# Optimization experiments

Hardware: AMD Instinct MI355X
Metric: run time of the kernel (lower is better)

The kernel has to match this reference:

```python
import jax, jax.numpy as jnp
import numpy as np

DECAY = 0.8
COMMITMENT_WEIGHT = 1.0
EPS = 1e-5


def setup_inputs() -> dict:
    key = jax.random.key(0)
    k1, k2, k3 = jax.random.split(key, 3)
    B, T, D, K = 16, 2048, 512, 8192
    x = jax.random.normal(k1, (B, T, D), dtype=jnp.float32)
    embed = jax.random.normal(k2, (D, K), dtype=jnp.float32)
    cluster_size = jnp.ones((K,), dtype=jnp.float32)
    embed_avg = jax.random.normal(k3, (D, K), dtype=jnp.float32)
    return {"x": x, "embed": embed, "cluster_size": cluster_size, "embed_avg": embed_avg}


def reference(x, embed, cluster_size, embed_avg):
    B, T, D = x.shape
    K = embed.shape[1]
    flat = x.reshape(-1, D)  # [N, D]

    # squared L2 distance to each code: ||f||^2 - 2 f.e + ||e||^2  -> [N, K]
    dist = (flat * flat).sum(-1, keepdims=True) \
        - 2.0 * (flat @ embed) \
        + (embed * embed).sum(0, keepdims=True)
    embed_ind = jnp.argmin(dist, axis=1)  # [N] (== argmax of -dist)

    quantize = jnp.take(embed.T, embed_ind, axis=0).reshape(B, T, D)

    # ---- EMA codebook statistics (training-mode buffer updates) ----
    onehot_sum = jnp.zeros((K,), dtype=flat.dtype).at[embed_ind].add(1.0)  # [K]
    # flat.T @ onehot == segment-sum of tokens per code, transposed -> [D, K]
    embed_sum = jax.ops.segment_sum(flat, embed_ind, num_segments=K).T
    new_cluster_size = cluster_size * DECAY + (1.0 - DECAY) * onehot_sum
    new_embed_avg = embed_avg * DECAY + (1.0 - DECAY) * embed_sum
    n = new_cluster_size.sum()
    cs = (new_cluster_size + EPS) / (n + K * EPS) * n
    new_embed = new_embed_avg / cs[None, :]
    # (random re-init of unused codes is omitted: non-deterministic side effect)

    commitment_loss = jnp.mean((jax.lax.stop_gradient(quantize) - x) ** 2) * COMMITMENT_WEIGHT
    quantize_st = x + jax.lax.stop_gradient(quantize - x)  # straight-through

    return (quantize_st, embed_ind.reshape(B, T), commitment_loss,
            new_embed, new_cluster_size, new_embed_avg)
```

## Files before the change

kernel.cpp:

```cpp
#include <hip/hip_runtime.h>

#define NTOK   32768
#define DDIM   512
#define KCODES 8192
#define DK     (DDIM * KCODES)
#define DECAYF 0.8f
#define EPSF   1e-5f

using short8 = __attribute__((ext_vector_type(8))) short;
using f32x4  = __attribute__((ext_vector_type(4))) float;

#define WS_ESUMT  0
#define WS_ONEHOT DK
#define WS_ENORM  (DK + 8192)
#define WS_SCAL   (DK + 16384)
#define WS_PART   (WS_SCAL + 64)
#define WS_EHI    (WS_PART + 2 * NTOK)
#define WS_ELO    (WS_EHI + DK / 2)

__device__ __forceinline__ unsigned short bf16rne(float f) {
  unsigned u = __float_as_uint(f);
  unsigned r = u + 0x7FFFu + ((u >> 16) & 1u);
  return (unsigned short)(r >> 16);
}

__device__ __forceinline__ void gload_lds16(const unsigned short* g, unsigned short* l) {
  __builtin_amdgcn_global_load_lds(
      (const __attribute__((address_space(1))) unsigned int*)g,
      (__attribute__((address_space(3))) unsigned int*)l, 16, 0, 0);
}

__global__ __launch_bounds__(256) void prep_kernel(
    const float* __restrict__ x, const float* __restrict__ embed,
    const float* __restrict__ cluster_size,
    unsigned short* __restrict__ xhi, unsigned short* __restrict__ xlo,
    unsigned short* __restrict__ ehi, unsigned short* __restrict__ elo,
    float* __restrict__ e_norm, float* __restrict__ esumT,
    float* __restrict__ onehot, float* __restrict__ scal,
    unsigned long long* __restrict__ partials) {
  __shared__ float tile[32][33];
  __shared__ float part[8][32];
  __shared__ float w[4];
  const int bid = blockIdx.x;
  const int tid = threadIdx.x;

  if (bid < 8192) {
    const size_t i = ((size_t)bid * 256 + tid) * 8;
    const float4 v0 = *(const float4*)&x[i];
    const float4 v1 = *(const float4*)&x[i + 4];
    const float v[8] = {v0.x, v0.y, v0.z, v0.w, v1.x, v1.y, v1.z, v1.w};
    unsigned short h[8], l[8];
#pragma unroll
    for (int j = 0; j < 8; ++j) {
      h[j] = bf16rne(v[j]);
      l[j] = bf16rne(v[j] - __uint_as_float((unsigned)h[j] << 16));
    }
    uint4 H, L;
    H.x = h[0] | ((unsigned)h[1] << 16); H.y = h[2] | ((unsigned)h[3] << 16);
    H.z = h[4] | ((unsigned)h[5] << 16); H.w = h[6] | ((unsigned)h[7] << 16);
    L.x = l[0] | ((unsigned)l[1] << 16); L.y = l[2] | ((unsigned)l[3] << 16);
    L.z = l[4] | ((unsigned)l[5] << 16); L.w = l[6] | ((unsigned)l[7] << 16);
    *(uint4*)&xhi[i] = H;
    *(uint4*)&xlo[i] = L;
  } else if (bid < 8192 + 256) {
    const int k0 = (bid - 8192) * 32;
    const int tx = tid & 31;
    const int ty = tid >> 5;
    float sq = 0.f;
#pragma unroll 1
    for (int d0 = 0; d0 < DDIM; d0 += 32) {
      __syncthreads();
#pragma unroll
      for (int j = 0; j < 4; ++j) {
        const int dl = ty + j * 8;
        const float v = embed[(size_t)(d0 + dl) * KCODES + k0 + tx];
        tile[dl][tx] = v;
        sq += v * v;
      }
      __syncthreads();
#pragma unroll
      for (int j = 0; j < 4; ++j) {
        const int kl = ty + j * 8;
        const size_t idx = (size_t)(k0 + kl) * DDIM + d0 + tx;
        const float v = tile[tx][kl];
        const unsigned short h = bf16rne(v);
        ehi[idx] = h;
        elo[idx] = bf16rne(v - __uint_as_float((unsigned)h << 16));
      }
    }
    part[ty][tx] = sq;
    __syncthreads();
    if (ty == 0) {
      float s = 0.f;
#pragma unroll
      for (int j = 0; j < 8; ++j) s += part[j][tx];
      e_norm[k0 + tx] = s;
    }
  } else if (bid < 8192 + 256 + 2048) {
    const int zb = bid - (8192 + 256);
    const size_t off = (size_t)zb * 2048 + (size_t)tid * 8;
    const float4 z = {0.f, 0.f, 0.f, 0.f};
    *(float4*)&esumT[off] = z;
    *(float4*)&esumT[off + 4] = z;
  } else {
    const int b = bid - (8192 + 256 + 2048);
    onehot[b * 256 + tid] = 0.f;
    const size_t pbase = (size_t)b * 1024 + (size_t)tid * 4;
    const ulonglong2 ff = {~0ull, ~0ull};
    *(ulonglong2*)&partials[pbase] = ff;
    *(ulonglong2*)&partials[pbase + 2] = ff;
    float s = cluster_size[b * 256 + tid];
#pragma unroll
    for (int off = 32; off > 0; off >>= 1) s += __shfl_down(s, off);
    if ((tid & 63) == 0) w[tid >> 6] = s;
    __syncthreads();
    if (tid == 0) {
      scal[2 + b] = w[0] + w[1] + w[2] + w[3];
      if (b == 0) { scal[0] = 0.f; scal[1] = 0.f; }
    }
  }
}

__global__ __launch_bounds__(256) void argmin_mfma_kernel(
    const unsigned short* __restrict__ xhi, const unsigned short* __restrict__ xlo,
    const unsigned short* __restrict__ ehi, const unsigned short* __restrict__ elo,
    const float* __restrict__ e_norm, unsigned long long* __restrict__ partials) {
  __shared__ unsigned short Ahs[128 * 32];
  __shared__ unsigned short Als[128 * 32];
  __shared__ unsigned short Bhs[128 * 32];
  __shared__ unsigned short Bls[128 * 32];

  const int t    = threadIdx.x;
  const int wid  = t >> 6;
  const int lid  = t & 63;
  const int kblk = blockIdx.x;
  const int tokbase = blockIdx.y * 128;
  const int kbase   = kblk * 128;

  const int wrow = wid >> 1, wcol = wid & 1;
  const int m16  = lid & 15, kq = lid >> 4;

  const int srow = lid >> 2;
  const int gcol = ((lid & 3) ^ ((srow >> 1) & 3)) * 8;
  const int fsw = (kq ^ ((m16 >> 1) & 3)) * 8;

  f32x4 acc[4][4];
#pragma unroll
  for (int i = 0; i < 4; ++i)
#pragma unroll
    for (int j = 0; j < 4; ++j) acc[i][j] = (f32x4)0.f;

  const unsigned short* Ahg = xhi + (size_t)tokbase * DDIM;
  const unsigned short* Alg = xlo + (size_t)tokbase * DDIM;
  const unsigned short* Bhg = ehi + (size_t)kbase * DDIM;
  const unsigned short* Blg = elo + (size_t)kbase * DDIM;

#pragma unroll 1
  for (int d0 = 0; d0 < DDIM; d0 += 32) {
    __syncthreads();
#pragma unroll
    for (int p = 0; p < 2; ++p) {
      const int chunk = wid + p * 4;
      const size_t go = (size_t)(chunk * 16 + srow) * DDIM + d0 + gcol;
      gload_lds16(Ahg + go, &Ahs[chunk * 512]);
      gload_lds16(Alg + go, &Als[chunk * 512]);
      gload_lds16(Bhg + go, &Bhs[chunk * 512]);
      gload_lds16(Blg + go, &Bls[chunk * 512]);
    }
    __syncthreads();
    short8 bh[4], bl[4];
#pragma unroll
    for (int j = 0; j < 4; ++j) {
      const int r = (wcol * 64 + j * 16 + m16) * 32 + fsw;
      bh[j] = *(const short8*)&Bhs[r];
      bl[j] = *(const short8*)&Bls[r];
    }
#pragma unroll
    for (int i = 0; i < 4; ++i) {
      const int r = (wrow * 64 + i * 16 + m16) * 32 + fsw;
      const short8 ah = *(const short8*)&Ahs[r];
      const short8 al = *(const short8*)&Als[r];
#pragma unroll
      for (int j = 0; j < 4; ++j) {
        acc[i][j] = __builtin_amdgcn_mfma_f32_16x16x32_bf16(ah, bh[j], acc[i][j], 0, 0, 0);
        acc[i][j] = __builtin_amdgcn_mfma_f32_16x16x32_bf16(ah, bl[j], acc[i][j], 0, 0, 0);
        acc[i][j] = __builtin_amdgcn_mfma_f32_16x16x32_bf16(al, bh[j], acc[i][j], 0, 0, 0);
      }
    }
  }

  float en[4];
#pragma unroll
  for (int j = 0; j < 4; ++j)
    en[j] = e_norm[kbase + wcol * 64 + j * 16 + m16];

  __syncthreads();
  unsigned long long* red = (unsigned long long*)Ahs;
#pragma unroll
  for (int i = 0; i < 4; ++i) {
#pragma unroll
    for (int r = 0; r < 4; ++r) {
      unsigned long long best = 0xFFFFFFFFFFFFFFFFull;
#pragma unroll
      for (int j = 0; j < 4; ++j) {
        const float s = en[j] - 2.0f * acc[i][j][r];
        unsigned u = __float_as_uint(s);
        u = (u & 0x80000000u) ? ~u : (u | 0x80000000u);
        const unsigned k = (unsigned)(kbase + wcol * 64 + j * 16 + m16);
        const unsigned long long c = ((unsigned long long)u << 32) | k;
        best = (c < best) ? c : best;
      }
#pragma unroll
      for (int s = 1; s < 16; s <<= 1) {
        const unsigned long long c = __shfl_xor(best, s);
        best = (c < best) ? c : best;
      }
      if (m16 == 0)
        red[(wrow * 64 + i * 16 + kq * 4 + r) * 2 + wcol] = best;
    }
  }
  __syncthreads();
  if (t < 128) {
    const unsigned long long a0 = red[t * 2], a1 = red[t * 2 + 1];
    const unsigned long long m = (a0 < a1) ? a0 : a1;
    atomicMin(&partials[tokbase + t], m);
  }
}

__global__ __launch_bounds__(256) void gather_stats_kernel(
    const float* __restrict__ x, const unsigned short* __restrict__ ehi,
    const unsigned short* __restrict__ elo,
    const unsigned long long* __restrict__ partials,
    float* __restrict__ quant_out, float* __restrict__ indf_out,
    float* __restrict__ embed_sumT, float* __restrict__ onehot,
    float* __restrict__ scal) {
  const int sub = threadIdx.x >> 7;
  const int t7  = threadIdx.x & 127;
  const int n   = blockIdx.x * 2 + sub;
  __shared__ int s_ind[2];
  __shared__ float wsum[4];
  if (t7 == 0) {
    const int k = (int)(partials[n] & 0xFFFFFFFFull);
    s_ind[sub] = k;
    indf_out[n] = (float)k;
    atomicAdd(&onehot[k], 1.0f);
  }
  __syncthreads();
  const int k = s_ind[sub];
  const int d4 = t7 * 4;
  const ushort4 h4 = *(const ushort4*)&ehi[(size_t)k * DDIM + d4];
  const ushort4 l4 = *(const ushort4*)&elo[(size_t)k * DDIM + d4];
  float4 e;
  e.x = __uint_as_float((unsigned)h4.x << 16) + __uint_as_float((unsigned)l4.x << 16);
  e.y = __uint_as_float((unsigned)h4.y << 16) + __uint_as_float((unsigned)l4.y << 16);
  e.z = __uint_as_float((unsigned)h4.z << 16) + __uint_as_float((unsigned)l4.z << 16);
  e.w = __uint_as_float((unsigned)h4.w << 16) + __uint_as_float((unsigned)l4.w << 16);
  const float4 xv = *(const float4*)&x[(size_t)n * DDIM + d4];
  *(float4*)&quant_out[(size_t)n * DDIM + d4] = e;
  atomicAdd(&embed_sumT[(size_t)k * DDIM + d4 + 0], xv.x);
  atomicAdd(&embed_sumT[(size_t)k * DDIM + d4 + 1], xv.y);
  atomicAdd(&embed_sumT[(size_t)k * DDIM + d4 + 2], xv.z);
  atomicAdd(&embed_sumT[(size_t)k * DDIM + d4 + 3], xv.w);
  const float dx0 = e.x - xv.x, dx1 = e.y - xv.y, dx2 = e.z - xv.z, dx3 = e.w - xv.w;
  float ls = dx0 * dx0 + dx1 * dx1 + dx2 * dx2 + dx3 * dx3;
#pragma unroll
  for (int off = 32; off > 0; off >>= 1) ls += __shfl_down(ls, off);
  if ((threadIdx.x & 63) == 0) wsum[threadIdx.x >> 6] = ls;
  __syncthreads();
  if (threadIdx.x == 0)
    atomicAdd(&scal[0], wsum[0] + wsum[1] + wsum[2] + wsum[3]);
}

__global__ __launch_bounds__(256) void finalize_kernel(
    const float* __restrict__ embed_avg, const float* __restrict__ embed_sumT,
    const float* __restrict__ cluster_size, const float* __restrict__ onehot,
    const float* __restrict__ scal,
    float* __restrict__ out_embed, float* __restrict__ out_avg,
    float* __restrict__ out_ncs, float* __restrict__ out_loss) {
  __shared__ float tile[32][33];
  __shared__ float sh_nsum;
  const int k0 = blockIdx.x * 32;
  const int d0 = blockIdx.y * 32;
  const int tx = threadIdx.x & 31;
  const int ty = threadIdx.x >> 5;
  if (threadIdx.x == 0) {
    float s = 0.f;
#pragma unroll
    for (int b = 0; b < 32; ++b) s += scal[2 + b];
    sh_nsum = DECAYF * s + (1.0f - DECAYF) * (float)NTOK;
  }
#pragma unroll
  for (int j = 0; j < 4; ++j) {
    const int kl = ty + j * 8;
    tile[kl][tx] = embed_sumT[(size_t)(k0 + kl) * DDIM + d0 + tx];
  }
  __syncthreads();
  const float nsum = sh_nsum;
  const float ncs = DECAYF * cluster_size[k0 + tx] + (1.0f - DECAYF) * onehot[k0 + tx];
  const float csv = (ncs + EPSF) / (nsum + (float)KCODES * EPSF) * nsum;
#pragma unroll
  for (int j = 0; j < 4; ++j) {
    const int dl = ty + j * 8;
    const size_t idx = (size_t)(d0 + dl) * KCODES + k0 + tx;
    const float nea = DECAYF * embed_avg[idx] + (1.0f - DECAYF) * tile[tx][dl];
    out_avg[idx] = nea;
    out_embed[idx] = nea / csv;
  }
  if (blockIdx.y == 0 && ty == 0)
    out_ncs[k0 + tx] = ncs;
  if (blockIdx.x == 0 && blockIdx.y == 0 && threadIdx.x == 0)
    out_loss[0] = scal[0] * (1.0f / ((float)NTOK * (float)DDIM));
}

extern "C" void kernel_launch(void* const* d_in, const int* in_sizes, int n_in,
                              void* d_out, int out_size, void* d_ws, size_t ws_size,
                              hipStream_t stream) {
  (void)in_sizes; (void)n_in; (void)out_size; (void)ws_size;
  const float* x            = (const float*)d_in[0];
  const float* embed        = (const float*)d_in[1];
  const float* cluster_size = (const float*)d_in[2];
  const float* embed_avg    = (const float*)d_in[3];

  float* out = (float*)d_out;
  float* out_quant = out;
  float* out_indf  = out + 16777216;
  float* out_loss  = out + 16777216 + 32768;
  float* out_embed = out + 16777216 + 32768 + 1;
  float* out_ncs   = out_embed + DK;
  float* out_avg   = out_ncs + KCODES;

  float* ws = (float*)d_ws;
  float* esumT  = ws + WS_ESUMT;
  float* onehot = ws + WS_ONEHOT;
  float* e_norm = ws + WS_ENORM;
  float* scal   = ws + WS_SCAL;
  unsigned long long* partials = (unsigned long long*)(ws + WS_PART);
  unsigned short* ehi = (unsigned short*)(ws + WS_EHI);
  unsigned short* elo = (unsigned short*)(ws + WS_ELO);

  unsigned short* xhi = (unsigned short*)d_out;
  unsigned short* xlo = xhi + (size_t)NTOK * DDIM;

  prep_kernel<<<8192 + 256 + 2048 + 32, 256, 0, stream>>>(
      x, embed, cluster_size, xhi, xlo, ehi, elo, e_norm, esumT, onehot, scal, partials);

  argmin_mfma_kernel<<<dim3(64, 256), 256, 0, stream>>>(
      xhi, xlo, ehi, elo, e_norm, partials);

  gather_stats_kernel<<<NTOK / 2, 256, 0, stream>>>(
      x, ehi, elo, partials, out_quant, out_indf, esumT, onehot, scal);

  finalize_kernel<<<dim3(KCODES / 32, DDIM / 32), 256, 0, stream>>>(
      embed_avg, esumT, cluster_size, onehot, scal,
      out_embed, out_avg, out_ncs, out_loss);
}
```

Before: 1.382 ms.

## Fuse gather/stats into argmin via last-block counter; move quantize write to finalize

```diff
diff --git a/kernel.cpp b/kernel.cpp
--- a/kernel.cpp
+++ b/kernel.cpp
@@ -14,7 +14,8 @@
 #define WS_ONEHOT DK
 #define WS_ENORM  (DK + 8192)
 #define WS_SCAL   (DK + 16384)
-#define WS_PART   (WS_SCAL + 64)
+#define WS_CNT    (WS_SCAL + 64)
+#define WS_PART   (WS_CNT + 256)
 #define WS_EHI    (WS_PART + 2 * NTOK)
 #define WS_ELO    (WS_EHI + DK / 2)
 
@@ -22,6 +23,10 @@
   unsigned u = __float_as_uint(f);
   unsigned r = u + 0x7FFFu + ((u >> 16) & 1u);
   return (unsigned short)(r >> 16);
+}
+
+__device__ __forceinline__ float bf2f(unsigned short h) {
+  return __uint_as_float((unsigned)h << 16);
 }
 
 __device__ __forceinline__ void gload_lds16(const unsigned short* g, unsigned short* l) {
@@ -37,7 +42,7 @@
     unsigned short* __restrict__ ehi, unsigned short* __restrict__ elo,
     float* __restrict__ e_norm, float* __restrict__ esumT,
     float* __restrict__ onehot, float* __restrict__ scal,
-    unsigned long long* __restrict__ partials) {
+    unsigned* __restrict__ cnt, unsigned long long* __restrict__ partials) {
   __shared__ float tile[32][33];
   __shared__ float part[8][32];
   __shared__ float w[4];
@@ -53,7 +58,7 @@
 #pragma unroll
     for (int j = 0; j < 8; ++j) {
       h[j] = bf16rne(v[j]);
-      l[j] = bf16rne(v[j] - __uint_as_float((unsigned)h[j] << 16));
+      l[j] = bf16rne(v[j] - bf2f(h[j]));
     }
     uint4 H, L;
     H.x = h[0] | ((unsigned)h[1] << 16); H.y = h[2] | ((unsigned)h[3] << 16);
@@ -85,7 +90,7 @@
         const float v = tile[tx][kl];
         const unsigned short h = bf16rne(v);
         ehi[idx] = h;
-        elo[idx] = bf16rne(v - __uint_as_float((unsigned)h << 16));
+        elo[idx] = bf16rne(v - bf2f(h));
       }
     }
     part[ty][tx] = sq;
@@ -109,6 +114,7 @@
     const ulonglong2 ff = {~0ull, ~0ull};
     *(ulonglong2*)&partials[pbase] = ff;
     *(ulonglong2*)&partials[pbase + 2] = ff;
+    if (b == 0) cnt[tid] = 0u;
     float s = cluster_size[b * 256 + tid];
 #pragma unroll
     for (int off = 32; off > 0; off >>= 1) s += __shfl_down(s, off);
@@ -124,7 +130,10 @@
 __global__ __launch_bounds__(256) void argmin_mfma_kernel(
     const unsigned short* __restrict__ xhi, const unsigned short* __restrict__ xlo,
     const unsigned short* __restrict__ ehi, const unsigned short* __restrict__ elo,
-    const float* __restrict__ e_norm, unsigned long long* __restrict__ partials) {
+    const float* __restrict__ e_norm, unsigned long long* __restrict__ partials,
+    const float* __restrict__ x, float* __restrict__ indf_out,
+    float* __restrict__ onehot, float* __restrict__ esumT,
+    float* __restrict__ scal, unsigned* __restrict__ cnt) {
   __shared__ unsigned short Ahs[128 * 32];
   __shared__ unsigned short Als[128 * 32];
   __shared__ unsigned short Bhs[128 * 32];
@@ -225,64 +234,91 @@
     const unsigned long long m = (a0 < a1) ? a0 : a1;
     atomicMin(&partials[tokbase + t], m);
   }
-}
-
-__global__ __launch_bounds__(256) void gather_stats_kernel(
-    const float* __restrict__ x, const unsigned short* __restrict__ ehi,
-    const unsigned short* __restrict__ elo,
-    const unsigned long long* __restrict__ partials,
-    float* __restrict__ quant_out, float* __restrict__ indf_out,
-    float* __restrict__ embed_sumT, float* __restrict__ onehot,
-    float* __restrict__ scal) {
-  const int sub = threadIdx.x >> 7;
-  const int t7  = threadIdx.x & 127;
-  const int n   = blockIdx.x * 2 + sub;
-  __shared__ int s_ind[2];
-  __shared__ float wsum[4];
-  if (t7 == 0) {
-    const int k = (int)(partials[n] & 0xFFFFFFFFull);
-    s_ind[sub] = k;
-    indf_out[n] = (float)k;
-    atomicAdd(&onehot[k], 1.0f);
-  }
-  __syncthreads();
-  const int k = s_ind[sub];
-  const int d4 = t7 * 4;
-  const ushort4 h4 = *(const ushort4*)&ehi[(size_t)k * DDIM + d4];
-  const ushort4 l4 = *(const ushort4*)&elo[(size_t)k * DDIM + d4];
-  float4 e;
-  e.x = __uint_as_float((unsigned)h4.x << 16) + __uint_as_float((unsigned)l4.x << 16);
-  e.y = __uint_as_float((unsigned)h4.y << 16) + __uint_as_float((unsigned)l4.y << 16);
-  e.z = __uint_as_float((unsigned)h4.z << 16) + __uint_as_float((unsigned)l4.z << 16);
-  e.w = __uint_as_float((unsigned)h4.w << 16) + __uint_as_float((unsigned)l4.w << 16);
-  const float4 xv = *(const float4*)&x[(size_t)n * DDIM + d4];
-  *(float4*)&quant_out[(size_t)n * DDIM + d4] = e;
-  atomicAdd(&embed_sumT[(size_t)k * DDIM + d4 + 0], xv.x);
-  atomicAdd(&embed_sumT[(size_t)k * DDIM + d4 + 1], xv.y);
-  atomicAdd(&embed_sumT[(size_t)k * DDIM + d4 + 2], xv.z);
-  atomicAdd(&embed_sumT[(size_t)k * DDIM + d4 + 3], xv.w);
-  const float dx0 = e.x - xv.x, dx1 = e.y - xv.y, dx2 = e.z - xv.z, dx3 = e.w - xv.w;
-  float ls = dx0 * dx0 + dx1 * dx1 + dx2 * dx2 + dx3 * dx3;
-#pragma unroll
-  for (int off = 32; off > 0; off >>= 1) ls += __shfl_down(ls, off);
-  if ((threadIdx.x & 63) == 0) wsum[threadIdx.x >> 6] = ls;
-  __syncthreads();
-  if (threadIdx.x == 0)
-    atomicAdd(&scal[0], wsum[0] + wsum[1] + wsum[2] + wsum[3]);
+
+  __threadfence();
+  __syncthreads();
+  int* s_last = (int*)Als;
+  float* gred = (float*)(Als + 16);
+  if (t == 0) {
+    const unsigned v = atomicAdd(&cnt[blockIdx.y], 1u);
+    *s_last = (v == 63u);
+  }
+  __syncthreads();
+  if (*s_last) {
+    __threadfence();
+    float ls = 0.f;
+#pragma unroll 1
+    for (int i = 0; i < 32; ++i) {
+      const int n = tokbase + i * 4 + wid;
+      unsigned long long pv = 0ull;
+      if (lid == 0) pv = atomicAdd(&partials[n], 0ull);
+      int k = (int)(pv & 0xFFFFFFFFull);
+      k = __shfl(k, 0);
+      if (lid == 0) {
+        indf_out[n] = (float)k;
+        atomicAdd(&onehot[k], 1.0f);
+      }
+      const int d8 = lid * 8;
+      const float4 xv0 = *(const float4*)&x[(size_t)n * DDIM + d8];
+      const float4 xv1 = *(const float4*)&x[(size_t)n * DDIM + d8 + 4];
+      const ushort4 h0 = *(const ushort4*)&ehi[(size_t)k * DDIM + d8];
+      const ushort4 h1 = *(const ushort4*)&ehi[(size_t)k * DDIM + d8 + 4];
+      const ushort4 l0 = *(const ushort4*)&elo[(size_t)k * DDIM + d8];
+      const ushort4 l1 = *(const ushort4*)&elo[(size_t)k * DDIM + d8 + 4];
+      const float xv[8] = {xv0.x, xv0.y, xv0.z, xv0.w, xv1.x, xv1.y, xv1.z, xv1.w};
+      const float ev[8] = {
+          bf2f(h0.x) + bf2f(l0.x), bf2f(h0.y) + bf2f(l0.y),
+          bf2f(h0.z) + bf2f(l0.z), bf2f(h0.w) + bf2f(l0.w),
+          bf2f(h1.x) + bf2f(l1.x), bf2f(h1.y) + bf2f(l1.y),
+          bf2f(h1.z) + bf2f(l1.z), bf2f(h1.w) + bf2f(l1.w)};
+#pragma unroll
+      for (int j = 0; j < 8; ++j) {
+        atomicAdd(&esumT[(size_t)k * DDIM + d8 + j], xv[j]);
+        const float dx = ev[j] - xv[j];
+        ls += dx * dx;
+      }
+    }
+#pragma unroll
+    for (int off = 32; off > 0; off >>= 1) ls += __shfl_down(ls, off);
+    if (lid == 0) gred[wid] = ls;
+    __syncthreads();
+    if (t == 0) atomicAdd(&scal[0], gred[0] + gred[1] + gred[2] + gred[3]);
+  }
 }
 
 __global__ __launch_bounds__(256) void finalize_kernel(
     const float* __restrict__ embed_avg, const float* __restrict__ embed_sumT,
     const float* __restrict__ cluster_size, const float* __restrict__ onehot,
-    const float* __restrict__ scal,
+    const float* __restrict__ scal, const unsigned long long* __restrict__ partials,
+    const unsigned short* __restrict__ ehi, const unsigned short* __restrict__ elo,
     float* __restrict__ out_embed, float* __restrict__ out_avg,
-    float* __restrict__ out_ncs, float* __restrict__ out_loss) {
+    float* __restrict__ out_ncs, float* __restrict__ out_loss,
+    float* __restrict__ out_quant) {
   __shared__ float tile[32][33];
   __shared__ float sh_nsum;
   const int k0 = blockIdx.x * 32;
   const int d0 = blockIdx.y * 32;
   const int tx = threadIdx.x & 31;
   const int ty = threadIdx.x >> 5;
+
+  {
+    const int nbase = (blockIdx.y * 256 + blockIdx.x) * 8;
+    const int n = nbase + (threadIdx.x >> 5);
+    const int k = (int)(partials[n] & 0xFFFFFFFFull);
+    const int d16 = (threadIdx.x & 31) * 16;
+#pragma unroll
+    for (int c = 0; c < 4; ++c) {
+      const ushort4 h4 = *(const ushort4*)&ehi[(size_t)k * DDIM + d16 + c * 4];
+      const ushort4 l4 = *(const ushort4*)&elo[(size_t)k * DDIM + d16 + c * 4];
+      float4 e;
+      e.x = bf2f(h4.x) + bf2f(l4.x);
+      e.y = bf2f(h4.y) + bf2f(l4.y);
+      e.z = bf2f(h4.z) + bf2f(l4.z);
+      e.w = bf2f(h4.w) + bf2f(l4.w);
+      *(float4*)&out_quant[(size_t)n * DDIM + d16 + c * 4] = e;
+    }
+  }
+
   if (threadIdx.x == 0) {
     float s = 0.f;
 #pragma unroll
@@ -334,6 +370,7 @@
   float* onehot = ws + WS_ONEHOT;
   float* e_norm = ws + WS_ENORM;
   float* scal   = ws + WS_SCAL;
+  unsigned* cnt = (unsigned*)(ws + WS_CNT);
   unsigned long long* partials = (unsigned long long*)(ws + WS_PART);
   unsigned short* ehi = (unsigned short*)(ws + WS_EHI);
   unsigned short* elo = (unsigned short*)(ws + WS_ELO);
@@ -342,15 +379,14 @@
   unsigned short* xlo = xhi + (size_t)NTOK * DDIM;
 
   prep_kernel<<<8192 + 256 + 2048 + 32, 256, 0, stream>>>(
-      x, embed, cluster_size, xhi, xlo, ehi, elo, e_norm, esumT, onehot, scal, partials);
+      x, embed, cluster_size, xhi, xlo, ehi, elo, e_norm, esumT, onehot, scal,
+      cnt, partials);
 
   argmin_mfma_kernel<<<dim3(64, 256), 256, 0, stream>>>(
-      xhi, xlo, ehi, elo, e_norm, partials);
-
-  gather_stats_kernel<<<NTOK / 2, 256, 0, stream>>>(
-      x, ehi, elo, partials, out_quant, out_indf, esumT, onehot, scal);
+      xhi, xlo, ehi, elo, e_norm, partials,
+      x, out_indf, onehot, esumT, scal, cnt);
 
   finalize_kernel<<<dim3(KCODES / 32, DDIM / 32), 256, 0, stream>>>(
-      embed_avg, esumT, cluster_size, onehot, scal,
-      out_embed, out_avg, out_ncs, out_loss);
-}
+      embed_avg, esumT, cluster_size, onehot, scal, partials, ehi, elo,
+      out_embed, out_avg, out_ncs, out_loss, out_quant);
+}
```

Result: slower. 4.013 ms (+190.4%).
